# Optimization experiments

Hardware: AMD Instinct MI355X
Metric: run time of the kernel (lower is better)

Reference implementation:

```python
import jax, jax.numpy as jnp
import numpy as np

RADIUS = 0.4
K = 32
EPS = 1e-5


def ball_query(xyz, new_xyz, radius, k):
    """xyz: (B,N,3), new_xyz: (B,M,3) -> idx (B,M,k) int32.
    Replicates CUDA ball_query: first k points within radius (in index order),
    padded with the first found index."""
    N = xyz.shape[1]
    # squared distances (B,M,N)
    d2 = jnp.sum((new_xyz[:, :, None, :] - xyz[:, None, :, :]) ** 2, axis=-1)
    within = d2 < radius * radius
    order = jnp.arange(N, dtype=jnp.int32)
    key = jnp.where(within, order[None, None, :], N)
    idx_sorted = jnp.argsort(key, axis=-1)[..., :k].astype(jnp.int32)  # (B,M,k)
    cnt = within.sum(axis=-1)  # (B,M)
    first = idx_sorted[..., :1]
    slot = jnp.arange(k)[None, None, :]
    return jnp.where(slot < cnt[..., None], idx_sorted, first)


def gather_bmk(x_bnc, idx):
    """x_bnc: (B,N,C), idx: (B,M,K) -> (B,M,K,C)"""
    return jnp.take_along_axis(x_bnc[:, None, :, :], idx[..., None], axis=2)


def conv_bn_relu(x, w, b, gamma, beta):
    """x: (B,Cin,M,K); w: (Cout,Cin). 1x1 Conv2d + BatchNorm2d (train stats) + ReLU."""
    x = jnp.einsum('bcmk,oc->bomk', x, w) + b[None, :, None, None]
    mu = x.mean(axis=(0, 2, 3), keepdims=True)
    var = x.var(axis=(0, 2, 3), keepdims=True)
    x = gamma[None, :, None, None] * (x - mu) * jax.lax.rsqrt(var + EPS) + beta[None, :, None, None]
    return jax.nn.relu(x)


def setup_inputs() -> dict:
    key = jax.random.key(0)
    ks = jax.random.split(key, 16)
    B, N, C, M = 4, 16384, 128, 1024
    mlp = [131, 128, 128, 256]
    inp = {
        'points_xyz': jax.random.normal(ks[0], (B, N, 3), dtype=jnp.float32),
        'features': jax.random.normal(ks[1], (B, C, N), dtype=jnp.float32),
        'indices': jax.random.randint(ks[2], (B, M), 0, N, dtype=jnp.int32),
    }
    for i in range(3):
        cin, cout = mlp[i], mlp[i + 1]
        inp[f'w{i+1}'] = jax.random.normal(ks[3 + 4 * i], (cout, cin), dtype=jnp.float32) / np.sqrt(cin)
        inp[f'b{i+1}'] = jnp.zeros((cout,), dtype=jnp.float32)
        inp[f'g{i+1}'] = jnp.ones((cout,), dtype=jnp.float32)
        inp[f'beta{i+1}'] = jnp.zeros((cout,), dtype=jnp.float32)
    return inp


def reference(points_xyz, features, indices,
              w1, b1, g1, beta1, w2, b2, g2, beta2, w3, b3, g3, beta3):
    # sample centers: new_xyz (B,M,3)
    new_xyz = jnp.take_along_axis(points_xyz, indices[..., None], axis=1)
    # ball query + group
    idx = ball_query(points_xyz, new_xyz, RADIUS, K)            # (B,M,K)
    grouped_xyz = gather_bmk(points_xyz, idx) - new_xyz[:, :, None, :]  # (B,M,K,3)
    grouped_feat = gather_bmk(features.transpose(0, 2, 1), idx)         # (B,M,K,C)
    x = jnp.concatenate([grouped_xyz, grouped_feat], axis=-1)           # (B,M,K,3+C)
    x = x.transpose(0, 3, 1, 2)                                         # (B,3+C,M,K)
    # shared MLP (1x1 Conv2d + BN + ReLU)
    x = conv_bn_relu(x, w1, b1, g1, beta1)
    x = conv_bn_relu(x, w2, b2, g2, beta2)
    x = conv_bn_relu(x, w3, b3, g3, beta3)
    # max pool over K -> (B, Cout, M)
    new_features = x.max(axis=-1)
    return new_xyz, new_features
```

## Files before the change

kernel.cpp:

```cpp
#include <hip/hip_runtime.h>

#define B_ 4
#define N_ 16384
#define C_ 128
#define M_ 1024
#define K_ 32
#define NTOT (B_*M_*K_)
#define RAD2 0.16f
#define EPS_ 1e-5f

typedef unsigned short ushort_t;
typedef __bf16 bf16x8 __attribute__((ext_vector_type(8)));
typedef float f32x4 __attribute__((ext_vector_type(4)));

__device__ __forceinline__ float b2f(ushort_t u){
  unsigned int x = ((unsigned int)u) << 16;
  return __builtin_bit_cast(float, x);
}
__device__ __forceinline__ ushort_t f2b(float f){
  unsigned int u = __builtin_bit_cast(unsigned int, f);
  unsigned int r = (u + 0x7FFFu + ((u >> 16) & 1u)) >> 16;
  return (ushort_t)r;
}

__global__ __launch_bounds__(256) void ball_query_k(
    const float* __restrict__ xyz, const int* __restrict__ indices,
    float* __restrict__ new_xyz, int* __restrict__ idx)
{
  int t = threadIdx.x;
  int wv = t >> 6, lane = t & 63;
  int g = blockIdx.x*4 + wv;
  int b = g >> 10;
  const float* pb = xyz + (size_t)b*N_*3;
  const float4* pb4 = (const float4*)pb;
  int qi = indices[g];
  float qx = pb[qi*3+0], qy = pb[qi*3+1], qz = pb[qi*3+2];
  if (lane < 3) new_xyz[g*3 + lane] = pb[qi*3 + lane];

  int cnt = 0, firstIdx = 0;
  int* op = idx + g*K_;

  float4 buf0[6], buf1[6];
  #pragma unroll
  for (int i = 0; i < 6; i++) buf0[i] = pb4[lane*6 + i];

  auto process = [&](const float4* buf, int chunk){
    const float* f = (const float*)buf;
    unsigned int local_mask = 0;
    #pragma unroll
    for (int j = 0; j < 8; j++){
      float dx = f[j*3+0]-qx, dy = f[j*3+1]-qy, dz = f[j*3+2]-qz;
      if (dx*dx + dy*dy + dz*dz < RAD2) local_mask |= (1u << j);
    }
    if (__ballot(local_mask != 0) == 0ull) return;
    int base = chunk*512;
    int lcnt = __popc(local_mask);
    int incl = lcnt;
    #pragma unroll
    for (int d = 1; d < 64; d <<= 1){
      int tt = __shfl_up(incl, d);
      if (lane >= d) incl += tt;
    }
    int excl = incl - lcnt;
    int total = __shfl(incl, 63);
    if (cnt == 0){
      int lf = local_mask ? (lane*8 + __builtin_ctz(local_mask)) : 0x7fffffff;
      #pragma unroll
      for (int d = 1; d < 64; d <<= 1) lf = min(lf, __shfl_xor(lf, d));
      firstIdx = base + lf;
    }
    int sl = cnt + excl;
    unsigned int m = local_mask;
    while (m && sl < K_){
      int j = __builtin_ctz(m); m &= m - 1u;
      op[sl++] = base + lane*8 + j;
    }
    cnt += total;
  };

  for (int chunk = 0; chunk < 32; chunk += 2){
    if (chunk + 1 < 32){
      #pragma unroll
      for (int i = 0; i < 6; i++) buf1[i] = pb4[(chunk+1)*384 + lane*6 + i];
    }
    process(buf0, chunk);
    if (cnt >= K_) break;
    if (chunk + 2 < 32){
      #pragma unroll
      for (int i = 0; i < 6; i++) buf0[i] = pb4[(chunk+2)*384 + lane*6 + i];
    }
    process(buf1, chunk + 1);
    if (cnt >= K_) break;
  }
  if (cnt < K_){
    for (int s = cnt + lane; s < K_; s += 64) op[s] = firstIdx;
  }
}

__global__ __launch_bounds__(256) void transpose_feat_k(
    const float* __restrict__ feat, ushort_t* __restrict__ ftr_t)
{
  __shared__ float T[32][133];
  int bi = blockIdx.x;
  int b = bi >> 9, ntile = bi & 511;
  int n0 = ntile * 32;
  int t = threadIdx.x;
  int nl = t & 31;
  #pragma unroll
  for (int ci = 0; ci < 16; ci++){
    int c = ci*8 + (t >> 5);
    T[nl][c] = feat[((size_t)b*C_ + c)*N_ + n0 + nl];
  }
  __syncthreads();
  #pragma unroll
  for (int ii = 0; ii < 2; ii++){
    int v = ii*256 + t;
    int n2 = v >> 4, seg = v & 15;
    union { ushort_t u[8]; uint4 q; } pk;
    #pragma unroll
    for (int j = 0; j < 8; j++) pk.u[j] = f2b(T[n2][seg*8 + j]);
    *(uint4*)(ftr_t + ((size_t)b*N_ + n0 + n2)*C_ + seg*8) = pk.q;
  }
}

__global__ __launch_bounds__(256) void prep_w_k(
    const float* __restrict__ w1, const float* __restrict__ w2, const float* __restrict__ w3,
    ushort_t* __restrict__ W1b, ushort_t* __restrict__ W2b, ushort_t* __restrict__ W3b)
{
  const int T1 = 128*160, T2 = 128*128, T3 = 256*128;
  for (int e = blockIdx.x*256 + threadIdx.x; e < T1+T2+T3; e += gridDim.x*256){
    if (e < T1){
      int o = e / 160, c = e % 160;
      float v = 0.f;
      if (c < 128) v = w1[o*131 + 3 + c];
      else if (c < 131) v = w1[o*131 + (c - 128)];
      W1b[e] = f2b(v);
    } else if (e < T1+T2){
      int e2 = e - T1;
      W2b[e2] = f2b(w2[e2]);
    } else {
      int e3 = e - T1 - T2;
      W3b[e3] = f2b(w3[e3]);
    }
  }
}

__global__ __launch_bounds__(256, 2) void conv1_k(
    const float* __restrict__ xyz, const ushort_t* __restrict__ ftr_t,
    const int* __restrict__ idx, const float* __restrict__ new_xyz,
    const ushort_t* __restrict__ W1b, const float* __restrict__ b1,
    ushort_t* __restrict__ Y1, float* __restrict__ sumO, float* __restrict__ sqO)
{
  __shared__ alignas(16) ushort_t Xs[32*168];
  __shared__ alignas(16) float Ys[32*132];
  int t = threadIdx.x;
  int wv = t >> 6, lane = t & 63, quad = lane >> 4, l15 = lane & 15;
  int row = t >> 3, chunk = t & 7;

  if (t < 128){
    int rr = t >> 2, cc = t & 3;
    *(uint4*)(Xs + rr*168 + 128 + cc*8) = make_uint4(0,0,0,0);
  }
  bf16x8 wf[2][5];
  #pragma unroll
  for (int nt = 0; nt < 2; nt++)
    #pragma unroll
    for (int kt = 0; kt < 5; kt++)
      wf[nt][kt] = *(const bf16x8*)(W1b + (wv*32 + nt*16 + l15)*160 + kt*32 + quad*8);
  float bs_r[2] = { b1[wv*32 + l15], b1[wv*32 + 16 + l15] };
  float s[2] = {0.f,0.f}, s2[2] = {0.f,0.f};

  const int GPB = 8;
  int g0 = blockIdx.x * GPB;
  for (int i = 0; i < GPB; i++){
    int g = g0 + i;
    int b = g >> 10;
    int n = idx[g*K_ + row];
    const ushort_t* src = ftr_t + ((size_t)b*N_ + n)*C_ + chunk*16;
    uint4 q0 = *(const uint4*)src;
    uint4 q1 = *(const uint4*)(src + 8);
    *(uint4*)(Xs + row*168 + chunk*16) = q0;
    *(uint4*)(Xs + row*168 + chunk*16 + 8) = q1;
    if (t < 32){
      int n2 = idx[g*K_ + t];
      const float* pp = xyz + ((size_t)b*N_ + n2)*3;
      const float* qq = new_xyz + (size_t)g*3;
      unsigned int u0 = (unsigned int)f2b(pp[0]-qq[0]) | ((unsigned int)f2b(pp[1]-qq[1]) << 16);
      unsigned int u1 = (unsigned int)f2b(pp[2]-qq[2]);
      *(uint2*)(Xs + t*168 + 128) = make_uint2(u0, u1);
    }
    __syncthreads();
    bf16x8 af[2][5];
    #pragma unroll
    for (int mt = 0; mt < 2; mt++)
      #pragma unroll
      for (int kt = 0; kt < 5; kt++)
        af[mt][kt] = *(const bf16x8*)(Xs + (mt*16 + l15)*168 + kt*32 + quad*8);
    f32x4 acc[2][2];
    #pragma unroll
    for (int nt = 0; nt < 2; nt++){ acc[nt][0] = (f32x4){0,0,0,0}; acc[nt][1] = (f32x4){0,0,0,0}; }
    #pragma unroll
    for (int nt = 0; nt < 2; nt++)
      #pragma unroll
      for (int kt = 0; kt < 5; kt++){
        acc[nt][0] = __builtin_amdgcn_mfma_f32_16x16x32_bf16(af[0][kt], wf[nt][kt], acc[nt][0], 0,0,0);
        acc[nt][1] = __builtin_amdgcn_mfma_f32_16x16x32_bf16(af[1][kt], wf[nt][kt], acc[nt][1], 0,0,0);
      }
    #pragma unroll
    for (int nt = 0; nt < 2; nt++){
      int o = wv*32 + nt*16 + l15;
      #pragma unroll
      for (int mt = 0; mt < 2; mt++)
        #pragma unroll
        for (int r = 0; r < 4; r++){
          float v = acc[nt][mt][r] + bs_r[nt];
          s[nt] += v; s2[nt] += v*v;
          Ys[(mt*16 + quad*4 + r)*132 + o] = v;
        }
    }
    __syncthreads();
    {
      const float* yp = &Ys[row*132 + chunk*16];
      f32x4 y0 = *(const f32x4*)(yp);
      f32x4 y1 = *(const f32x4*)(yp + 4);
      f32x4 y2 = *(const f32x4*)(yp + 8);
      f32x4 y3 = *(const f32x4*)(yp + 12);
      union { ushort_t u[8]; uint4 q; } p0, p1;
      #pragma unroll
      for (int j = 0; j < 4; j++){
        p0.u[j] = f2b(y0[j]); p0.u[4+j] = f2b(y1[j]);
        p1.u[j] = f2b(y2[j]); p1.u[4+j] = f2b(y3[j]);
      }
      ushort_t* dst = Y1 + ((size_t)g*K_ + row)*128 + chunk*16;
      *(uint4*)dst = p0.q;
      *(uint4*)(dst + 8) = p1.q;
    }
  }
  #pragma unroll
  for (int nt = 0; nt < 2; nt++){
    s[nt]  += __shfl_xor(s[nt], 16);  s[nt]  += __shfl_xor(s[nt], 32);
    s2[nt] += __shfl_xor(s2[nt], 16); s2[nt] += __shfl_xor(s2[nt], 32);
    if (quad == 0){
      int o = wv*32 + nt*16 + l15;
      atomicAdd(&sumO[o], s[nt]);
      atomicAdd(&sqO[o], s2[nt]);
    }
  }
}

template<int COUT, bool MAXMIN>
__global__ __launch_bounds__(256, 2) void convB_k(
    const ushort_t* __restrict__ Yin, const ushort_t* __restrict__ Wb,
    const float* __restrict__ bias, const float* __restrict__ g_bn,
    const float* __restrict__ beta_bn, const float* __restrict__ sumI,
    const float* __restrict__ sqI, ushort_t* __restrict__ Yout,
    unsigned int* __restrict__ Ymm, float* __restrict__ sumO, float* __restrict__ sqO)
{
  constexpr int NT = COUT/64;
  __shared__ alignas(16) ushort_t Xs[32*136];
  __shared__ alignas(16) float Ys[MAXMIN ? 4 : 32*132];
  int t = threadIdx.x;
  int wv = t >> 6, lane = t & 63, quad = lane >> 4, l15 = lane & 15;
  int row = t >> 3, chunk = t & 7;

  float a_r[16], d_r[16];
  #pragma unroll
  for (int j = 0; j < 16; j++){
    int c = chunk*16 + j;
    float mu  = sumI[c] * (1.f/NTOT);
    float var = sqI[c]  * (1.f/NTOT) - mu*mu;
    float a = g_bn[c] * rsqrtf(var + EPS_);
    a_r[j] = a; d_r[j] = beta_bn[c] - a*mu;
  }
  bf16x8 wf[NT][4];
  #pragma unroll
  for (int nt = 0; nt < NT; nt++)
    #pragma unroll
    for (int kt = 0; kt < 4; kt++)
      wf[nt][kt] = *(const bf16x8*)(Wb + (wv*(NT*16) + nt*16 + l15)*128 + kt*32 + quad*8);
  float bs_r[NT];
  #pragma unroll
  for (int nt = 0; nt < NT; nt++) bs_r[nt] = bias[wv*(NT*16) + nt*16 + l15];
  float s[NT], s2[NT];
  #pragma unroll
  for (int nt = 0; nt < NT; nt++){ s[nt] = 0.f; s2[nt] = 0.f; }

  const int GPB = 8;
  int g0 = blockIdx.x * GPB;
  uint4 r0, r1;
  {
    const ushort_t* src = Yin + ((size_t)g0*K_ + row)*128 + chunk*16;
    r0 = *(const uint4*)src; r1 = *(const uint4*)(src + 8);
  }
  for (int i = 0; i < GPB; i++){
    int g = g0 + i;
    union { ushort_t u[8]; uint4 q; } i0, i1, o0, o1;
    i0.q = r0; i1.q = r1;
    #pragma unroll
    for (int j = 0; j < 8; j++){
      o0.u[j] = f2b(fmaxf(a_r[j]  *b2f(i0.u[j]) + d_r[j],   0.f));
      o1.u[j] = f2b(fmaxf(a_r[8+j]*b2f(i1.u[j]) + d_r[8+j], 0.f));
    }
    *(uint4*)(Xs + row*136 + chunk*16) = o0.q;
    *(uint4*)(Xs + row*136 + chunk*16 + 8) = o1.q;
    if (i + 1 < GPB){
      const ushort_t* src = Yin + ((size_t)(g+1)*K_ + row)*128 + chunk*16;
      r0 = *(const uint4*)src; r1 = *(const uint4*)(src + 8);
    }
    __syncthreads();
    bf16x8 af[2][4];
    #pragma unroll
    for (int mt = 0; mt < 2; mt++)
      #pragma unroll
      for (int kt = 0; kt < 4; kt++)
        af[mt][kt] = *(const bf16x8*)(Xs + (mt*16 + l15)*136 + kt*32 + quad*8);
    f32x4 acc[NT][2];
    #pragma unroll
    for (int nt = 0; nt < NT; nt++){ acc[nt][0] = (f32x4){0,0,0,0}; acc[nt][1] = (f32x4){0,0,0,0}; }
    #pragma unroll
    for (int nt = 0; nt < NT; nt++)
      #pragma unroll
      for (int kt = 0; kt < 4; kt++){
        acc[nt][0] = __builtin_amdgcn_mfma_f32_16x16x32_bf16(af[0][kt], wf[nt][kt], acc[nt][0], 0,0,0);
        acc[nt][1] = __builtin_amdgcn_mfma_f32_16x16x32_bf16(af[1][kt], wf[nt][kt], acc[nt][1], 0,0,0);
      }
    if constexpr (!MAXMIN){
      #pragma unroll
      for (int nt = 0; nt < NT; nt++){
        int o = wv*(NT*16) + nt*16 + l15;
        #pragma unroll
        for (int mt = 0; mt < 2; mt++)
          #pragma unroll
          for (int r = 0; r < 4; r++){
            float v = acc[nt][mt][r] + bs_r[nt];
            s[nt] += v; s2[nt] += v*v;
            Ys[(mt*16 + quad*4 + r)*132 + o] = v;
          }
      }
      __syncthreads();
      const float* yp = &Ys[row*132 + chunk*16];
      f32x4 y0 = *(const f32x4*)(yp);
      f32x4 y1 = *(const f32x4*)(yp + 4);
      f32x4 y2 = *(const f32x4*)(yp + 8);
      f32x4 y3 = *(const f32x4*)(yp + 12);
      union { ushort_t u[8]; uint4 q; } p0, p1;
      #pragma unroll
      for (int j = 0; j < 4; j++){
        p0.u[j] = f2b(y0[j]); p0.u[4+j] = f2b(y1[j]);
        p1.u[j] = f2b(y2[j]); p1.u[4+j] = f2b(y3[j]);
      }
      ushort_t* dst = Yout + ((size_t)g*K_ + row)*128 + chunk*16;
      *(uint4*)dst = p0.q;
      *(uint4*)(dst + 8) = p1.q;
    } else {
      #pragma unroll
      for (int nt = 0; nt < NT; nt++){
        float v0 = acc[nt][0][0] + bs_r[nt];
        float mx = v0, mn = v0;
        s[nt] += v0; s2[nt] += v0*v0;
        #pragma unroll
        for (int mt = 0; mt < 2; mt++)
          #pragma unroll
          for (int r = 0; r < 4; r++){
            if (mt == 0 && r == 0) continue;
            float v = acc[nt][mt][r] + bs_r[nt];
            s[nt] += v; s2[nt] += v*v;
            mx = fmaxf(mx, v); mn = fminf(mn, v);
          }
        mx = fmaxf(mx, __shfl_xor(mx, 16)); mx = fmaxf(mx, __shfl_xor(mx, 32));
        mn = fminf(mn, __shfl_xor(mn, 16)); mn = fminf(mn, __shfl_xor(mn, 32));
        if (quad == 0){
          int o = wv*64 + nt*16 + l15;
          Ymm[(size_t)g*256 + o] = (unsigned int)f2b(mx) | ((unsigned int)f2b(mn) << 16);
        }
      }
      __syncthreads();
    }
  }
  #pragma unroll
  for (int nt = 0; nt < NT; nt++){
    s[nt]  += __shfl_xor(s[nt], 16);  s[nt]  += __shfl_xor(s[nt], 32);
    s2[nt] += __shfl_xor(s2[nt], 16); s2[nt] += __shfl_xor(s2[nt], 32);
    if (quad == 0){
      int o = wv*(NT*16) + nt*16 + l15;
      atomicAdd(&sumO[o], s[nt]);
      atomicAdd(&sqO[o], s2[nt]);
    }
  }
}

__global__ __launch_bounds__(256) void finalize_k(
    const unsigned int* __restrict__ Ymm, const float* __restrict__ g3,
    const float* __restrict__ beta3, const float* __restrict__ sum3,
    const float* __restrict__ sq3, float* __restrict__ out)
{
  __shared__ float T[16][264];
  __shared__ float abn[256], dbn[256];
  int t = threadIdx.x;
  int b = blockIdx.x >> 6;
  int m0 = (blockIdx.x & 63) * 16;
  {
    float mu  = sum3[t] * (1.f/NTOT);
    float var = sq3[t]  * (1.f/NTOT) - mu*mu;
    float a = g3[t] * rsqrtf(var + EPS_);
    abn[t] = a; dbn[t] = beta3[t] - a*mu;
  }
  __syncthreads();
  #pragma unroll
  for (int i = 0; i < 4; i++){
    int v4 = i*256 + t;
    int m = v4 >> 6, oq = (v4 & 63) * 4;
    uint4 w = *(const uint4*)(Ymm + ((size_t)(b*M_ + m0 + m))*256 + oq);
    unsigned int wsv[4] = {w.x, w.y, w.z, w.w};
    float r[4];
    #pragma unroll
    for (int j = 0; j < 4; j++){
      int o = oq + j;
      float mx = b2f((ushort_t)(wsv[j] & 0xffffu));
      float mn = b2f((ushort_t)(wsv[j] >> 16));
      float a = abn[o];
      float val = (a >= 0.f) ? (a*mx + dbn[o]) : (a*mn + dbn[o]);
      r[j] = fmaxf(val, 0.f);
    }
    *(f32x4*)(&T[m][oq]) = *(f32x4*)r;
  }
  __syncthreads();
  #pragma unroll
  for (int p = 0; p < 4; p++){
    int o = p*64 + (t >> 2), c = t & 3;
    float4 v = make_float4(T[c*4+0][o], T[c*4+1][o], T[c*4+2][o], T[c*4+3][o]);
    *(float4*)(out + ((size_t)(b*256 + o))*M_ + m0 + c*4) = v;
  }
}

extern "C" void kernel_launch(void* const* d_in, const int* in_sizes, int n_in,
                              void* d_out, int out_size, void* d_ws, size_t ws_size,
                              hipStream_t stream)
{
  (void)in_sizes; (void)n_in; (void)out_size; (void)ws_size;
  const float* xyz  = (const float*)d_in[0];
  const float* feat = (const float*)d_in[1];
  const int*   inds = (const int*)d_in[2];
  const float* w1 = (const float*)d_in[3];
  const float* b1 = (const float*)d_in[4];
  const float* g1 = (const float*)d_in[5];
  const float* be1= (const float*)d_in[6];
  const float* w2 = (const float*)d_in[7];
  const float* b2 = (const float*)d_in[8];
  const float* g2 = (const float*)d_in[9];
  const float* be2= (const float*)d_in[10];
  const float* w3 = (const float*)d_in[11];
  const float* b3 = (const float*)d_in[12];
  const float* g3 = (const float*)d_in[13];
  const float* be3= (const float*)d_in[14];

  char* ws = (char*)d_ws;
  float* stats = (float*)ws;
  float* s1sum = stats + 0*256;  float* s1sq = stats + 1*256;
  float* s2sum = stats + 2*256;  float* s2sq = stats + 3*256;
  float* s3sum = stats + 4*256;  float* s3sq = stats + 5*256;
  size_t off = 6*256*sizeof(float);
  int* idx = (int*)(ws + off);                off += (size_t)B_*M_*K_*4;
  ushort_t* ftr_t = (ushort_t*)(ws + off);    off += (size_t)B_*N_*C_*2;
  ushort_t* W1b = (ushort_t*)(ws + off);      off += 128*160*2;
  ushort_t* W2b = (ushort_t*)(ws + off);      off += 128*128*2;
  ushort_t* W3b = (ushort_t*)(ws + off);      off += 256*128*2;
  ushort_t* Y1 = (ushort_t*)(ws + off);       off += (size_t)NTOT*128*2;
  ushort_t* Y2 = (ushort_t*)(ws + off);       off += (size_t)NTOT*128*2;
  unsigned int* Ymm = (unsigned int*)(ws + off); off += (size_t)B_*M_*256*4;

  float* new_xyz  = (float*)d_out;
  float* out_feat = (float*)d_out + (size_t)B_*M_*3;

  hipMemsetAsync(stats, 0, 6*256*sizeof(float), stream);
  prep_w_k<<<272, 256, 0, stream>>>(w1, w2, w3, W1b, W2b, W3b);
  transpose_feat_k<<<2048, 256, 0, stream>>>(feat, ftr_t);
  ball_query_k<<<1024, 256, 0, stream>>>(xyz, inds, new_xyz, idx);
  conv1_k<<<512, 256, 0, stream>>>(xyz, ftr_t, idx, new_xyz, W1b, b1, Y1, s1sum, s1sq);
  convB_k<128,false><<<512, 256, 0, stream>>>(Y1, W2b, b2, g1, be1, s1sum, s1sq, Y2, nullptr, s2sum, s2sq);
  convB_k<256,true ><<<512, 256, 0, stream>>>(Y2, W3b, b3, g2, be2, s2sum, s2sq, nullptr, Ymm, s3sum, s3sq);
  finalize_k<<<256, 256, 0, stream>>>(Ymm, g3, be3, s3sum, s3sq, out_feat);
}
```

Before: 227.6 us.

## Double-buffer LDS tiles, swap MFMA operands to store outputs directly, prefetch gathers

The conv1 and convB kernels now swap the MFMA operand order, so each lane holds four consecutive output channels for one row. Each lane can then write packed bf16 output straight to global memory, which removes the fp32 LDS staging buffer and one barrier per group. The input LDS tile is double-buffered so one barrier per iteration is enough. conv1 also preloads the gather indices and prefetches the next group's features and coordinates to overlap gather latency with compute. In exchange, global stores become narrower 8-byte writes spread across rows, and per-lane statistic accumulators grow four times, raising register pressure.

```diff
diff --git a/kernel.cpp b/kernel.cpp
--- a/kernel.cpp
+++ b/kernel.cpp
@@ -21,6 +21,9 @@
   unsigned int u = __builtin_bit_cast(unsigned int, f);
   unsigned int r = (u + 0x7FFFu + ((u >> 16) & 1u)) >> 16;
   return (ushort_t)r;
+}
+__device__ __forceinline__ unsigned int pack2(float a, float b){
+  return (unsigned int)f2b(a) | ((unsigned int)f2b(b) << 16);
 }
 
 __global__ __launch_bounds__(256) void ball_query_k(
@@ -151,15 +154,15 @@
     const ushort_t* __restrict__ W1b, const float* __restrict__ b1,
     ushort_t* __restrict__ Y1, float* __restrict__ sumO, float* __restrict__ sqO)
 {
-  __shared__ alignas(16) ushort_t Xs[32*168];
-  __shared__ alignas(16) float Ys[32*132];
+  __shared__ alignas(16) ushort_t Xs[2][32*168];
   int t = threadIdx.x;
   int wv = t >> 6, lane = t & 63, quad = lane >> 4, l15 = lane & 15;
   int row = t >> 3, chunk = t & 7;
 
   if (t < 128){
     int rr = t >> 2, cc = t & 3;
-    *(uint4*)(Xs + rr*168 + 128 + cc*8) = make_uint4(0,0,0,0);
+    *(uint4*)(&Xs[0][rr*168 + 128 + cc*8]) = make_uint4(0,0,0,0);
+    *(uint4*)(&Xs[1][rr*168 + 128 + cc*8]) = make_uint4(0,0,0,0);
   }
   bf16x8 wf[2][5];
   #pragma unroll
@@ -167,35 +170,47 @@
     #pragma unroll
     for (int kt = 0; kt < 5; kt++)
       wf[nt][kt] = *(const bf16x8*)(W1b + (wv*32 + nt*16 + l15)*160 + kt*32 + quad*8);
-  float bs_r[2] = { b1[wv*32 + l15], b1[wv*32 + 16 + l15] };
-  float s[2] = {0.f,0.f}, s2[2] = {0.f,0.f};
+  f32x4 bs4[2] = { *(const f32x4*)(b1 + wv*32 + quad*4),
+                   *(const f32x4*)(b1 + wv*32 + 16 + quad*4) };
+  float s[2][4] = {{0}}, s2[2][4] = {{0}};
 
   const int GPB = 8;
   int g0 = blockIdx.x * GPB;
+  int b = g0 >> 10;
+  int ia[GPB], ibv[GPB];
+  #pragma unroll
+  for (int i = 0; i < GPB; i++){
+    ia[i]  = idx[(g0+i)*K_ + row];
+    ibv[i] = idx[(g0+i)*K_ + (t & 31)];
+  }
+  uint4 f0, f1; float pxv=0, pyv=0, pzv=0, qxv=0, qyv=0, qzv=0;
+  auto prefetch = [&](int i){
+    const ushort_t* src = ftr_t + ((size_t)b*N_ + ia[i])*C_ + chunk*16;
+    f0 = *(const uint4*)src; f1 = *(const uint4*)(src + 8);
+    const float* pp = xyz + ((size_t)b*N_ + ibv[i])*3;
+    pxv = pp[0]; pyv = pp[1]; pzv = pp[2];
+    const float* qq = new_xyz + (size_t)(g0+i)*3;
+    qxv = qq[0]; qyv = qq[1]; qzv = qq[2];
+  };
+  prefetch(0);
   for (int i = 0; i < GPB; i++){
     int g = g0 + i;
-    int b = g >> 10;
-    int n = idx[g*K_ + row];
-    const ushort_t* src = ftr_t + ((size_t)b*N_ + n)*C_ + chunk*16;
-    uint4 q0 = *(const uint4*)src;
-    uint4 q1 = *(const uint4*)(src + 8);
-    *(uint4*)(Xs + row*168 + chunk*16) = q0;
-    *(uint4*)(Xs + row*168 + chunk*16 + 8) = q1;
+    ushort_t* X = Xs[i & 1];
+    *(uint4*)(X + row*168 + chunk*16) = f0;
+    *(uint4*)(X + row*168 + chunk*16 + 8) = f1;
     if (t < 32){
-      int n2 = idx[g*K_ + t];
-      const float* pp = xyz + ((size_t)b*N_ + n2)*3;
-      const float* qq = new_xyz + (size_t)g*3;
-      unsigned int u0 = (unsigned int)f2b(pp[0]-qq[0]) | ((unsigned int)f2b(pp[1]-qq[1]) << 16);
-      unsigned int u1 = (unsigned int)f2b(pp[2]-qq[2]);
-      *(uint2*)(Xs + t*168 + 128) = make_uint2(u0, u1);
-    }
+      unsigned int u0 = pack2(pxv - qxv, pyv - qyv);
+      unsigned int u1 = (unsigned int)f2b(pzv - qzv);
+      *(uint2*)(X + t*168 + 128) = make_uint2(u0, u1);
+    }
+    if (i + 1 < GPB) prefetch(i + 1);
     __syncthreads();
     bf16x8 af[2][5];
     #pragma unroll
     for (int mt = 0; mt < 2; mt++)
       #pragma unroll
       for (int kt = 0; kt < 5; kt++)
-        af[mt][kt] = *(const bf16x8*)(Xs + (mt*16 + l15)*168 + kt*32 + quad*8);
+        af[mt][kt] = *(const bf16x8*)(X + (mt*16 + l15)*168 + kt*32 + quad*8);
     f32x4 acc[2][2];
     #pragma unroll
     for (int nt = 0; nt < 2; nt++){ acc[nt][0] = (f32x4){0,0,0,0}; acc[nt][1] = (f32x4){0,0,0,0}; }
@@ -203,49 +218,37 @@
     for (int nt = 0; nt < 2; nt++)
       #pragma unroll
       for (int kt = 0; kt < 5; kt++){
-        acc[nt][0] = __builtin_amdgcn_mfma_f32_16x16x32_bf16(af[0][kt], wf[nt][kt], acc[nt][0], 0,0,0);
-        acc[nt][1] = __builtin_amdgcn_mfma_f32_16x16x32_bf16(af[1][kt], wf[nt][kt], acc[nt][1], 0,0,0);
+        acc[nt][0] = __builtin_amdgcn_mfma_f32_16x16x32_bf16(wf[nt][kt], af[0][kt], acc[nt][0], 0,0,0);
+        acc[nt][1] = __builtin_amdgcn_mfma_f32_16x16x32_bf16(wf[nt][kt], af[1][kt], acc[nt][1], 0,0,0);
       }
     #pragma unroll
-    for (int nt = 0; nt < 2; nt++){
-      int o = wv*32 + nt*16 + l15;
-      #pragma unroll
-      for (int mt = 0; mt < 2; mt++)
-        #pragma unroll
-        for (int r = 0; r < 4; r++){
-          float v = acc[nt][mt][r] + bs_r[nt];
-          s[nt] += v; s2[nt] += v*v;
-          Ys[(mt*16 + quad*4 + r)*132 + o] = v;
-        }
-    }
-    __syncthreads();
-    {
-      const float* yp = &Ys[row*132 + chunk*16];
-      f32x4 y0 = *(const f32x4*)(yp);
-      f32x4 y1 = *(const f32x4*)(yp + 4);
-      f32x4 y2 = *(const f32x4*)(yp + 8);
-      f32x4 y3 = *(const f32x4*)(yp + 12);
-      union { ushort_t u[8]; uint4 q; } p0, p1;
-      #pragma unroll
-      for (int j = 0; j < 4; j++){
-        p0.u[j] = f2b(y0[j]); p0.u[4+j] = f2b(y1[j]);
-        p1.u[j] = f2b(y2[j]); p1.u[4+j] = f2b(y3[j]);
+    for (int nt = 0; nt < 2; nt++)
+      #pragma unroll
+      for (int mt = 0; mt < 2; mt++){
+        float v0 = acc[nt][mt][0] + bs4[nt][0];
+        float v1 = acc[nt][mt][1] + bs4[nt][1];
+        float v2 = acc[nt][mt][2] + bs4[nt][2];
+        float v3 = acc[nt][mt][3] + bs4[nt][3];
+        s[nt][0] += v0; s2[nt][0] += v0*v0;
+        s[nt][1] += v1; s2[nt][1] += v1*v1;
+        s[nt][2] += v2; s2[nt][2] += v2*v2;
+        s[nt][3] += v3; s2[nt][3] += v3*v3;
+        ushort_t* dst = Y1 + ((size_t)g*K_ + mt*16 + l15)*128 + wv*32 + nt*16 + quad*4;
+        *(uint2*)dst = make_uint2(pack2(v0, v1), pack2(v2, v3));
       }
-      ushort_t* dst = Y1 + ((size_t)g*K_ + row)*128 + chunk*16;
-      *(uint4*)dst = p0.q;
-      *(uint4*)(dst + 8) = p1.q;
-    }
-  }
-  #pragma unroll
-  for (int nt = 0; nt < 2; nt++){
-    s[nt]  += __shfl_xor(s[nt], 16);  s[nt]  += __shfl_xor(s[nt], 32);
-    s2[nt] += __shfl_xor(s2[nt], 16); s2[nt] += __shfl_xor(s2[nt], 32);
-    if (quad == 0){
-      int o = wv*32 + nt*16 + l15;
-      atomicAdd(&sumO[o], s[nt]);
-      atomicAdd(&sqO[o], s2[nt]);
-    }
-  }
+  }
+  #pragma unroll
+  for (int nt = 0; nt < 2; nt++)
+    #pragma unroll
+    for (int r = 0; r < 4; r++){
+      float a = s[nt][r], q = s2[nt][r];
+      a += __shfl_xor(a,1); a += __shfl_xor(a,2); a += __shfl_xor(a,4); a += __shfl_xor(a,8);
+      q += __shfl_xor(q,1); q += __shfl_xor(q,2); q += __shfl_xor(q,4); q += __shfl_xor(q,8);
+      if (l15 == 0){
+        int o = wv*32 + nt*16 + quad*4 + r;
+        atomicAdd(&sumO[o], a); atomicAdd(&sqO[o], q);
+      }
+    }
 }
 
 template<int COUT, bool MAXMIN>
@@ -257,8 +260,7 @@
     unsigned int* __restrict__ Ymm, float* __restrict__ sumO, float* __restrict__ sqO)
 {
   constexpr int NT = COUT/64;
-  __shared__ alignas(16) ushort_t Xs[32*136];
-  __shared__ alignas(16) float Ys[MAXMIN ? 4 : 32*132];
+  __shared__ alignas(16) ushort_t Xs[2][32*136];
   int t = threadIdx.x;
   int wv = t >> 6, lane = t & 63, quad = lane >> 4, l15 = lane & 15;
   int row = t >> 3, chunk = t & 7;
@@ -278,12 +280,17 @@
     #pragma unroll
     for (int kt = 0; kt < 4; kt++)
       wf[nt][kt] = *(const bf16x8*)(Wb + (wv*(NT*16) + nt*16 + l15)*128 + kt*32 + quad*8);
-  float bs_r[NT];
-  #pragma unroll
-  for (int nt = 0; nt < NT; nt++) bs_r[nt] = bias[wv*(NT*16) + nt*16 + l15];
-  float s[NT], s2[NT];
-  #pragma unroll
-  for (int nt = 0; nt < NT; nt++){ s[nt] = 0.f; s2[nt] = 0.f; }
+  f32x4 bs4[NT]; float bs_l[NT];
+  #pragma unroll
+  for (int nt = 0; nt < NT; nt++){
+    if constexpr (!MAXMIN) bs4[nt] = *(const f32x4*)(bias + wv*(NT*16) + nt*16 + quad*4);
+    else                   bs_l[nt] = bias[wv*(NT*16) + nt*16 + l15];
+  }
+  float s[NT][4], s2[NT][4];
+  #pragma unroll
+  for (int nt = 0; nt < NT; nt++)
+    #pragma unroll
+    for (int r = 0; r < 4; r++){ s[nt][r] = 0.f; s2[nt][r] = 0.f; }
 
   const int GPB = 8;
   int g0 = blockIdx.x * GPB;
@@ -294,6 +301,7 @@
   }
   for (int i = 0; i < GPB; i++){
     int g = g0 + i;
+    ushort_t* X = Xs[i & 1];
     union { ushort_t u[8]; uint4 q; } i0, i1, o0, o1;
     i0.q = r0; i1.q = r1;
     #pragma unroll
@@ -301,8 +309,8 @@
       o0.u[j] = f2b(fmaxf(a_r[j]  *b2f(i0.u[j]) + d_r[j],   0.f));
       o1.u[j] = f2b(fmaxf(a_r[8+j]*b2f(i1.u[j]) + d_r[8+j], 0.f));
     }
-    *(uint4*)(Xs + row*136 + chunk*16) = o0.q;
-    *(uint4*)(Xs + row*136 + chunk*16 + 8) = o1.q;
+    *(uint4*)(X + row*136 + chunk*16) = o0.q;
+    *(uint4*)(X + row*136 + chunk*16 + 8) = o1.q;
     if (i + 1 < GPB){
       const ushort_t* src = Yin + ((size_t)(g+1)*K_ + row)*128 + chunk*16;
       r0 = *(const uint4*)src; r1 = *(const uint4*)(src + 8);
@@ -313,58 +321,53 @@
     for (int mt = 0; mt < 2; mt++)
       #pragma unroll
       for (int kt = 0; kt < 4; kt++)
-        af[mt][kt] = *(const bf16x8*)(Xs + (mt*16 + l15)*136 + kt*32 + quad*8);
+        af[mt][kt] = *(const bf16x8*)(X + (mt*16 + l15)*136 + kt*32 + quad*8);
     f32x4 acc[NT][2];
     #pragma unroll
     for (int nt = 0; nt < NT; nt++){ acc[nt][0] = (f32x4){0,0,0,0}; acc[nt][1] = (f32x4){0,0,0,0}; }
-    #pragma unroll
-    for (int nt = 0; nt < NT; nt++)
-      #pragma unroll
-      for (int kt = 0; kt < 4; kt++){
-        acc[nt][0] = __builtin_amdgcn_mfma_f32_16x16x32_bf16(af[0][kt], wf[nt][kt], acc[nt][0], 0,0,0);
-        acc[nt][1] = __builtin_amdgcn_mfma_f32_16x16x32_bf16(af[1][kt], wf[nt][kt], acc[nt][1], 0,0,0);
-      }
     if constexpr (!MAXMIN){
       #pragma unroll
+      for (int nt = 0; nt < NT; nt++)
+        #pragma unroll
+        for (int kt = 0; kt < 4; kt++){
+          acc[nt][0] = __builtin_amdgcn_mfma_f32_16x16x32_bf16(wf[nt][kt], af[0][kt], acc[nt][0], 0,0,0);
+          acc[nt][1] = __builtin_amdgcn_mfma_f32_16x16x32_bf16(wf[nt][kt], af[1][kt], acc[nt][1], 0,0,0);
+        }
+      #pragma unroll
+      for (int nt = 0; nt < NT; nt++)
+        #pragma unroll
+        for (int mt = 0; mt < 2; mt++){
+          float v0 = acc[nt][mt][0] + bs4[nt][0];
+          float v1 = acc[nt][mt][1] + bs4[nt][1];
+          float v2 = acc[nt][mt][2] + bs4[nt][2];
+          float v3 = acc[nt][mt][3] + bs4[nt][3];
+          s[nt][0] += v0; s2[nt][0] += v0*v0;
+          s[nt][1] += v1; s2[nt][1] += v1*v1;
+          s[nt][2] += v2; s2[nt][2] += v2*v2;
+          s[nt][3] += v3; s2[nt][3] += v3*v3;
+          ushort_t* dst = Yout + ((size_t)g*K_ + mt*16 + l15)*128 + wv*(NT*16) + nt*16 + quad*4;
+          *(uint2*)dst = make_uint2(pack2(v0, v1), pack2(v2, v3));
+        }
+    } else {
+      #pragma unroll
+      for (int nt = 0; nt < NT; nt++)
+        #pragma unroll
+        for (int kt = 0; kt < 4; kt++){
+          acc[nt][0] = __builtin_amdgcn_mfma_f32_16x16x32_bf16(af[0][kt], wf[nt][kt], acc[nt][0], 0,0,0);
+          acc[nt][1] = __builtin_amdgcn_mfma_f32_16x16x32_bf16(af[1][kt], wf[nt][kt], acc[nt][1], 0,0,0);
+        }
+      #pragma unroll
       for (int nt = 0; nt < NT; nt++){
-        int o = wv*(NT*16) + nt*16 + l15;
-        #pragma unroll
-        for (int mt = 0; mt < 2; mt++)
-          #pragma unroll
-          for (int r = 0; r < 4; r++){
-            float v = acc[nt][mt][r] + bs_r[nt];
-            s[nt] += v; s2[nt] += v*v;
-            Ys[(mt*16 + quad*4 + r)*132 + o] = v;
-          }
-      }
-      __syncthreads();
-      const float* yp = &Ys[row*132 + chunk*16];
-      f32x4 y0 = *(const f32x4*)(yp);
-      f32x4 y1 = *(const f32x4*)(yp + 4);
-      f32x4 y2 = *(const f32x4*)(yp + 8);
-      f32x4 y3 = *(const f32x4*)(yp + 12);
-      union { ushort_t u[8]; uint4 q; } p0, p1;
-      #pragma unroll
-      for (int j = 0; j < 4; j++){
-        p0.u[j] = f2b(y0[j]); p0.u[4+j] = f2b(y1[j]);
-        p1.u[j] = f2b(y2[j]); p1.u[4+j] = f2b(y3[j]);
-      }
-      ushort_t* dst = Yout + ((size_t)g*K_ + row)*128 + chunk*16;
-      *(uint4*)dst = p0.q;
-      *(uint4*)(dst + 8) = p1.q;
-    } else {
-      #pragma unroll
-      for (int nt = 0; nt < NT; nt++){
-        float v0 = acc[nt][0][0] + bs_r[nt];
+        float v0 = acc[nt][0][0] + bs_l[nt];
         float mx = v0, mn = v0;
-        s[nt] += v0; s2[nt] += v0*v0;
+        s[nt][0] += v0; s2[nt][0] += v0*v0;
         #pragma unroll
         for (int mt = 0; mt < 2; mt++)
           #pragma unroll
           for (int r = 0; r < 4; r++){
             if (mt == 0 && r == 0) continue;
-            float v = acc[nt][mt][r] + bs_r[nt];
-            s[nt] += v; s2[nt] += v*v;
+            float v = acc[nt][mt][r] + bs_l[nt];
+            s[nt][0] += v; s2[nt][0] += v*v;
             mx = fmaxf(mx, v); mn = fminf(mn, v);
           }
         mx = fmaxf(mx, __shfl_xor(mx, 16)); mx = fmaxf(mx, __shfl_xor(mx, 32));
@@ -374,17 +377,31 @@
           Ymm[(size_t)g*256 + o] = (unsigned int)f2b(mx) | ((unsigned int)f2b(mn) << 16);
         }
       }
-      __syncthreads();
-    }
-  }
-  #pragma unroll
-  for (int nt = 0; nt < NT; nt++){
-    s[nt]  += __shfl_xor(s[nt], 16);  s[nt]  += __shfl_xor(s[nt], 32);
-    s2[nt] += __shfl_xor(s2[nt], 16); s2[nt] += __shfl_xor(s2[nt], 32);
-    if (quad == 0){
-      int o = wv*(NT*16) + nt*16 + l15;
-      atomicAdd(&sumO[o], s[nt]);
-      atomicAdd(&sqO[o], s2[nt]);
+    }
+  }
+  if constexpr (!MAXMIN){
+    #pragma unroll
+    for (int nt = 0; nt < NT; nt++)
+      #pragma unroll
+      for (int r = 0; r < 4; r++){
+        float a = s[nt][r], q = s2[nt][r];
+        a += __shfl_xor(a,1); a += __shfl_xor(a,2); a += __shfl_xor(a,4); a += __shfl_xor(a,8);
+        q += __shfl_xor(q,1); q += __shfl_xor(q,2); q += __shfl_xor(q,4); q += __shfl_xor(q,8);
+        if (l15 == 0){
+          int o = wv*(NT*16) + nt*16 + quad*4 + r;
+          atomicAdd(&sumO[o], a); atomicAdd(&sqO[o], q);
+        }
+      }
+  } else {
+    #pragma unroll
+    for (int nt = 0; nt < NT; nt++){
+      float a = s[nt][0], q = s2[nt][0];
+      a += __shfl_xor(a, 16); a += __shfl_xor(a, 32);
+      q += __shfl_xor(q, 16); q += __shfl_xor(q, 32);
+      if (quad == 0){
+        int o = wv*(NT*16) + nt*16 + l15;
+        atomicAdd(&sumO[o], a); atomicAdd(&sqO[o], q);
+      }
     }
   }
 }
```

Result: slower. 298.3 us (+31.0%).
